# Performance work log

Measured on AMD Instinct MI355X. Metric: run time of the kernel, lower is better.

## Reference

```python
import jax, jax.numpy as jnp
import numpy as np

N_NODES = 100000
N_EDGES = 320000
DIM = 256  # hidden_dim*2 (bi-RNN)
BN_EPS = 1e-5


def setup_inputs() -> dict:
    key = jax.random.key(0)
    k1, k2, k3 = jax.random.split(key, 3)
    x = jax.random.normal(k1, (N_NODES, DIM), dtype=jnp.float32)
    W = jax.random.normal(k2, (DIM, DIM), dtype=jnp.float32) * (1.0 / np.sqrt(DIM))
    b = jnp.zeros((DIM,), dtype=jnp.float32)
    gamma = jnp.ones((DIM,), dtype=jnp.float32)
    beta = jnp.zeros((DIM,), dtype=jnp.float32)
    edge_index = jax.random.randint(k3, (2, N_EDGES), 0, N_NODES, dtype=jnp.int64)
    return {"x": x, "W": W, "b": b, "gamma": gamma, "beta": beta,
            "edge_index": edge_index}


def reference(x, W, b, gamma, beta, edge_index):
    N = x.shape[0]
    # --- GCNConv: add self-loops, symmetric deg^-1/2 normalization ---
    loop = jnp.arange(N, dtype=edge_index.dtype)
    row = jnp.concatenate([edge_index[0], loop])  # source / j
    col = jnp.concatenate([edge_index[1], loop])  # target / i
    deg = jax.ops.segment_sum(jnp.ones_like(col, dtype=x.dtype), col,
                              num_segments=N)
    dinv = jax.lax.rsqrt(deg)  # deg >= 1 due to self-loops
    norm = dinv[row] * dinv[col]  # [E+N]
    h = x @ W  # linear transform before propagation (PyG GCNConv)
    msg = h[row] * norm[:, None]  # gather + scale, [E+N, F]
    out = jax.ops.segment_sum(msg, col, num_segments=N) + b  # scatter-add
    # --- BatchNorm1d over nodes (training-mode batch statistics) ---
    mean = jnp.mean(out, axis=0)
    var = jnp.var(out, axis=0)
    out = (out - mean) * jax.lax.rsqrt(var + BN_EPS) * gamma + beta
    return jnp.tanh(out)
```

## Files before the change

kernel.cpp:

```cpp
#include <hip/hip_runtime.h>
#include <stdint.h>

#define N_NODES 100000
#define N_EDGES 320000
#define DIM 256
#define BN_EPS 1e-5f

typedef __attribute__((ext_vector_type(8))) short short8;
typedef __attribute__((ext_vector_type(4))) float f32x4;
typedef __attribute__((ext_vector_type(2))) unsigned int u32x2;

__device__ __forceinline__ float bf2f(unsigned short u) {
    union { unsigned int i; float f; } v; v.i = ((unsigned int)u) << 16; return v.f;
}
__device__ __forceinline__ unsigned short f2bf(float f) {
    union { float f; unsigned int i; } v; v.f = f;
    unsigned int x = v.i;
    return (unsigned short)((x + 0x7fffu + ((x >> 16) & 1u)) >> 16);
}
__device__ __forceinline__ int eidx(const int* ei, int i64, int which, int e) {
    int idx = which * N_EDGES + e;
    return i64 ? ei[idx * 2] : ei[idx];
}
__device__ __forceinline__ f32x4 ldx4(const void* xv, int xf32, size_t off) {
    if (xf32) return *(const f32x4*)((const float*)xv + off);
    uint2 u = *(const uint2*)((const unsigned short*)xv + off);
    f32x4 o;
    o[0] = bf2f((unsigned short)(u.x & 0xffffu));
    o[1] = bf2f((unsigned short)(u.x >> 16));
    o[2] = bf2f((unsigned short)(u.y & 0xffffu));
    o[3] = bf2f((unsigned short)(u.y >> 16));
    return o;
}

__global__ void k_detect(const unsigned short* __restrict__ xs,
                         const unsigned short* __restrict__ wsw,
                         const int* __restrict__ ei, int* __restrict__ flags) {
    __shared__ int red[3];
    int tid = threadIdx.x;
    if (tid < 3) red[tid] = 0;
    __syncthreads();
    int badx = 0, badw = 0, nz = 0;
    for (int j = 0; j < 8; ++j) {
        if (!(fabsf(bf2f(xs[tid * 8 + j])) <= 1000.0f)) badx = 1;
        if (!(fabsf(bf2f(wsw[tid * 8 + j])) <= 1000.0f)) badw = 1;
        if (ei[(tid * 8 + j) * 2 + 1] != 0) nz = 1;
    }
    if (badx) atomicOr(&red[0], 1);
    if (badw) atomicOr(&red[1], 1);
    if (nz)   atomicOr(&red[2], 1);
    __syncthreads();
    if (tid == 0) { flags[0] = red[0]; flags[1] = red[1]; flags[2] = red[2] ? 0 : 1; }
}

__global__ void k_zero(int* __restrict__ cnt, float* __restrict__ stats) {
    int i = blockIdx.x * 256 + threadIdx.x;
    if (i < N_NODES) cnt[i] = 0;
    if (i < 512) stats[i] = 0.0f;
}

__global__ void k_cnt(const int* __restrict__ ei, int* __restrict__ cnt,
                      const int* __restrict__ flags) {
    int i64 = flags[2];
    int e = blockIdx.x * 256 + threadIdx.x;
    if (e < N_EDGES) atomicAdd(&cnt[eidx(ei, i64, 1, e)], 1);
}

__global__ void k_dinv(const int* __restrict__ cnt, float* __restrict__ dinv) {
    int i = blockIdx.x * 256 + threadIdx.x;
    if (i < N_NODES) dinv[i] = rsqrtf((float)cnt[i] + 1.0f);
}

__global__ void k_scan1(const int* __restrict__ cnt, int* __restrict__ partial) {
    __shared__ int red[256];
    int t = threadIdx.x, b = blockIdx.x;
    int i0 = b * 512 + t * 2;
    int s = 0;
    if (i0 < N_NODES) s += cnt[i0];
    if (i0 + 1 < N_NODES) s += cnt[i0 + 1];
    red[t] = s;
    __syncthreads();
    for (int off = 128; off > 0; off >>= 1) {
        if (t < off) red[t] += red[t + off];
        __syncthreads();
    }
    if (t == 0) partial[b] = red[0];
}

__global__ void k_scan2(const int* __restrict__ partial, int* __restrict__ pbase) {
    __shared__ int s[256];
    int t = threadIdx.x;
    int v = (t < 200) ? partial[t] : 0;
    s[t] = v;
    __syncthreads();
    for (int off = 1; off < 256; off <<= 1) {
        int u = (t >= off) ? s[t - off] : 0;
        __syncthreads();
        s[t] += u;
        __syncthreads();
    }
    if (t < 200) pbase[t] = s[t] - v;
}

__global__ void k_scan3(const int* __restrict__ cnt, const int* __restrict__ pbase,
                        int* __restrict__ row_start, int* __restrict__ cursor) {
    __shared__ int s[512];
    int t = threadIdx.x, b = blockIdx.x;
    int i = b * 512 + t;
    int v = (i < N_NODES) ? cnt[i] : 0;
    s[t] = v;
    __syncthreads();
    for (int off = 1; off < 512; off <<= 1) {
        int u = (t >= off) ? s[t - off] : 0;
        __syncthreads();
        s[t] += u;
        __syncthreads();
    }
    if (i < N_NODES) {
        int excl = pbase[b] + s[t] - v;
        row_start[i] = excl;
        cursor[i] = excl;
    }
}

__global__ void k_fill(const int* __restrict__ ei, const float* __restrict__ dinv,
                       int* __restrict__ cursor, int2* __restrict__ csr_pk,
                       const int* __restrict__ flags) {
    int i64 = flags[2];
    int e = blockIdx.x * 256 + threadIdx.x;
    if (e >= N_EDGES) return;
    int c = eidx(ei, i64, 1, e);
    int r = eidx(ei, i64, 0, e);
    int slot = atomicAdd(&cursor[c], 1);
    union { float f; int i; } u; u.f = dinv[r] * dinv[c];
    int2 pk; pk.x = r; pk.y = u.i;
    csr_pk[slot] = pk;
}

__global__ void k_wt(const void* __restrict__ wv, unsigned short* __restrict__ Wth,
                     unsigned short* __restrict__ Wtl, const int* __restrict__ flags) {
    int wf32 = flags[1];
    int k = blockIdx.x, n = threadIdx.x;
    float v = wf32 ? ((const float*)wv)[k * DIM + n]
                   : bf2f(((const unsigned short*)wv)[k * DIM + n]);
    unsigned short h = f2bf(v);
    Wth[(size_t)n * DIM + k] = h;
    Wtl[(size_t)n * DIM + k] = f2bf(v - bf2f(h));
}

__global__ void k_agg(const void* __restrict__ xv, const int* __restrict__ row_start,
                      const int* __restrict__ cnt, const int2* __restrict__ csr_pk,
                      const float* __restrict__ dinv,
                      unsigned short* __restrict__ zh, unsigned short* __restrict__ zl,
                      const int* __restrict__ flags, int base) {
    int xf32 = flags[0];
    int gid = blockIdx.x * 256 + threadIdx.x;
    int node = base + (gid >> 6);
    int lane = gid & 63;
    int start = row_start[node];
    int len = cnt[node];
    float dv = dinv[node];
    float s = dv * dv;

    int myi = node;
    float myn = 0.0f;
    if (lane < len) {
        int2 pk = csr_pk[start + lane];
        myi = pk.x;
        union { int i; float f; } u; u.i = pk.y;
        myn = u.f;
    }
    bool big = (len > 63);
    int n_eff;
    if (!big) {
        if (lane == len) myn = s;
        n_eff = len + 1;
    } else {
        n_eff = 64;
    }
    int npad = (n_eff + 3) & ~3;

    f32x4 acc = (f32x4){0.f, 0.f, 0.f, 0.f};
    size_t lo4 = (size_t)(lane * 4);

    if (xf32) {
        const float* xp = (const float*)xv;
        for (int j = 0; j < npad; j += 4) {
            int i0 = __shfl(myi, j),     i1 = __shfl(myi, j + 1);
            int i2 = __shfl(myi, j + 2), i3 = __shfl(myi, j + 3);
            float n0 = __shfl(myn, j),     n1 = __shfl(myn, j + 1);
            float n2 = __shfl(myn, j + 2), n3 = __shfl(myn, j + 3);
            f32x4 x0 = *(const f32x4*)(xp + (size_t)i0 * DIM + lo4);
            f32x4 x1 = *(const f32x4*)(xp + (size_t)i1 * DIM + lo4);
            f32x4 x2 = *(const f32x4*)(xp + (size_t)i2 * DIM + lo4);
            f32x4 x3 = *(const f32x4*)(xp + (size_t)i3 * DIM + lo4);
            #pragma unroll
            for (int q = 0; q < 4; ++q)
                acc[q] += n0 * x0[q] + n1 * x1[q] + n2 * x2[q] + n3 * x3[q];
        }
    } else {
        const unsigned short* xp = (const unsigned short*)xv;
        for (int j = 0; j < npad; j += 4) {
            int i0 = __shfl(myi, j),     i1 = __shfl(myi, j + 1);
            int i2 = __shfl(myi, j + 2), i3 = __shfl(myi, j + 3);
            float n0 = __shfl(myn, j),     n1 = __shfl(myn, j + 1);
            float n2 = __shfl(myn, j + 2), n3 = __shfl(myn, j + 3);
            uint2 u0 = *(const uint2*)(xp + (size_t)i0 * DIM + lo4);
            uint2 u1 = *(const uint2*)(xp + (size_t)i1 * DIM + lo4);
            uint2 u2 = *(const uint2*)(xp + (size_t)i2 * DIM + lo4);
            uint2 u3 = *(const uint2*)(xp + (size_t)i3 * DIM + lo4);
            acc[0] += n0 * bf2f((unsigned short)(u0.x & 0xffffu))
                    + n1 * bf2f((unsigned short)(u1.x & 0xffffu))
                    + n2 * bf2f((unsigned short)(u2.x & 0xffffu))
                    + n3 * bf2f((unsigned short)(u3.x & 0xffffu));
            acc[1] += n0 * bf2f((unsigned short)(u0.x >> 16))
                    + n1 * bf2f((unsigned short)(u1.x >> 16))
                    + n2 * bf2f((unsigned short)(u2.x >> 16))
                    + n3 * bf2f((unsigned short)(u3.x >> 16));
            acc[2] += n0 * bf2f((unsigned short)(u0.y & 0xffffu))
                    + n1 * bf2f((unsigned short)(u1.y & 0xffffu))
                    + n2 * bf2f((unsigned short)(u2.y & 0xffffu))
                    + n3 * bf2f((unsigned short)(u3.y & 0xffffu));
            acc[3] += n0 * bf2f((unsigned short)(u0.y >> 16))
                    + n1 * bf2f((unsigned short)(u1.y >> 16))
                    + n2 * bf2f((unsigned short)(u2.y >> 16))
                    + n3 * bf2f((unsigned short)(u3.y >> 16));
        }
    }
    if (big) {
        f32x4 xs = ldx4(xv, xf32, (size_t)node * DIM + lo4);
        #pragma unroll
        for (int q = 0; q < 4; ++q) acc[q] += s * xs[q];
        for (int t = 64; t < len; ++t) {
            int2 pk = csr_pk[start + t];
            union { int i; float f; } u; u.i = pk.y;
            f32x4 xr = ldx4(xv, xf32, (size_t)pk.x * DIM + lo4);
            #pragma unroll
            for (int q = 0; q < 4; ++q) acc[q] += u.f * xr[q];
        }
    }

    unsigned short h0 = f2bf(acc[0]), h1 = f2bf(acc[1]);
    unsigned short h2 = f2bf(acc[2]), h3 = f2bf(acc[3]);
    u32x2 vh, vl;
    vh[0] = (unsigned int)h0 | ((unsigned int)h1 << 16);
    vh[1] = (unsigned int)h2 | ((unsigned int)h3 << 16);
    vl[0] = (unsigned int)f2bf(acc[0] - bf2f(h0))
          | ((unsigned int)f2bf(acc[1] - bf2f(h1)) << 16);
    vl[1] = (unsigned int)f2bf(acc[2] - bf2f(h2))
          | ((unsigned int)f2bf(acc[3] - bf2f(h3)) << 16);
    size_t zo = (size_t)(node - base) * DIM + lane * 4;
    __builtin_nontemporal_store(vh, (u32x2*)(zh + zo));
    __builtin_nontemporal_store(vl, (u32x2*)(zl + zo));
}

__device__ __forceinline__ void stage_q(const char* zhB, const char* zlB,
                                        char* zsb, int q, int m0l, int tid) {
    #pragma unroll
    for (int i = 0; i < 5; ++i) {
        int d    = i * 4096 + tid * 16;
        int row  = d >> 8;
        int rem  = d & 255;
        int hl   = rem >> 7;
        int slot = (rem >> 4) & 7;
        int slog = slot ^ (row & 7);
        const char* srcb = hl ? zlB : zhB;
        size_t soff = (size_t)(m0l + row) * 512 + (size_t)(q * 128 + slog * 16);
        __builtin_amdgcn_global_load_lds(
            (const __attribute__((address_space(1))) unsigned int*)(srcb + soff),
            (__attribute__((address_space(3))) unsigned int*)(zsb + d),
            16, 0, 0);
    }
}

__launch_bounds__(256, 3)
__global__ void k_gemm(const unsigned short* __restrict__ zh,
                       const unsigned short* __restrict__ zl,
                       const unsigned short* __restrict__ Wth,
                       const unsigned short* __restrict__ Wtl,
                       float* __restrict__ out, float* __restrict__ stats, int base) {
    __shared__ char zs[2][20480];
    int tid = threadIdx.x;
    int m0l = blockIdx.x * 80;
    int w = tid >> 6, lane = tid & 63, quad = lane >> 4, rl = lane & 15;

    f32x4 acc[5][4];
    #pragma unroll
    for (int ms = 0; ms < 5; ++ms)
        #pragma unroll
        for (int nt = 0; nt < 4; ++nt)
            acc[ms][nt] = (f32x4){0.f, 0.f, 0.f, 0.f};

    const char* zhB = (const char*)zh;
    const char* zlB = (const char*)zl;

    stage_q(zhB, zlB, zs[0], 0, m0l, tid);
    __syncthreads();

    for (int q = 0; q < 4; ++q) {
        int cur = q & 1;
        if (q < 3) stage_q(zhB, zlB, zs[cur ^ 1], q + 1, m0l, tid);

        const char* zb = zs[cur];
        #pragma unroll
        for (int kk2 = 0; kk2 < 2; ++kk2) {
            int k0g = q * 64 + kk2 * 32 + quad * 8;
            short8 bh[4], bl[4];
            #pragma unroll
            for (int nt = 0; nt < 4; ++nt) {
                int n = w * 64 + nt * 16 + rl;
                bh[nt] = *(const short8*)(Wth + (size_t)n * DIM + k0g);
                bl[nt] = *(const short8*)(Wtl + (size_t)n * DIM + k0g);
            }
            #pragma unroll
            for (int ms = 0; ms < 5; ++ms) {
                int row = ms * 16 + rl;
                int sp  = (((kk2 * 4 + quad) ^ (row & 7)) << 4);
                const char* rb = zb + row * 256;
                short8 ah = *(const short8*)(rb + sp);
                short8 al = *(const short8*)(rb + 128 + sp);
                #pragma unroll
                for (int nt = 0; nt < 4; ++nt) {
                    acc[ms][nt] = __builtin_amdgcn_mfma_f32_16x16x32_bf16(ah, bh[nt], acc[ms][nt], 0, 0, 0);
                    acc[ms][nt] = __builtin_amdgcn_mfma_f32_16x16x32_bf16(al, bh[nt], acc[ms][nt], 0, 0, 0);
                    acc[ms][nt] = __builtin_amdgcn_mfma_f32_16x16x32_bf16(ah, bl[nt], acc[ms][nt], 0, 0, 0);
                }
            }
        }
        __syncthreads();
    }

    #pragma unroll
    for (int nt = 0; nt < 4; ++nt) {
        int col = w * 64 + nt * 16 + rl;
        float s1 = 0.f, s2 = 0.f;
        #pragma unroll
        for (int ms = 0; ms < 5; ++ms)
            #pragma unroll
            for (int i = 0; i < 4; ++i) {
                float v = acc[ms][nt][i];
                s1 += v; s2 += v * v;
                out[(size_t)(base + m0l + ms * 16 + quad * 4 + i) * DIM + col] = v;
            }
        s1 += __shfl_xor(s1, 16); s1 += __shfl_xor(s1, 32);
        s2 += __shfl_xor(s2, 16); s2 += __shfl_xor(s2, 32);
        if (lane < 16) {
            atomicAdd(&stats[col], s1);
            atomicAdd(&stats[256 + col], s2);
        }
    }
}

__global__ void k_fin(const float* __restrict__ stats, const void* __restrict__ gv,
                      const void* __restrict__ bv, float* __restrict__ scsh,
                      const int* __restrict__ flags) {
    int ff32 = flags[0];
    int f = threadIdx.x;
    const float invN = 1.0f / (float)N_NODES;
    float mean = stats[f] * invN;
    float var = stats[256 + f] * invN - mean * mean;
    float g = ff32 ? ((const float*)gv)[f] : bf2f(((const unsigned short*)gv)[f]);
    float bb = ff32 ? ((const float*)bv)[f] : bf2f(((const unsigned short*)bv)[f]);
    float sc = g * rsqrtf(var + BN_EPS);
    scsh[f] = sc;
    scsh[256 + f] = bb - mean * sc;
}

__global__ void k_final(float* __restrict__ out, const float* __restrict__ scsh) {
    int t = blockIdx.x * 256 + threadIdx.x;
    int f0 = (t & 63) * 4;
    size_t off = (size_t)t * 4;
    f32x4 v = *(const f32x4*)(out + off);
    f32x4 o;
    #pragma unroll
    for (int j = 0; j < 4; ++j)
        o[j] = tanhf(v[j] * scsh[f0 + j] + scsh[256 + f0 + j]);
    *(f32x4*)(out + off) = o;
}

extern "C" void kernel_launch(void* const* d_in, const int* in_sizes, int n_in,
                              void* d_out, int out_size, void* d_ws, size_t ws_size,
                              hipStream_t stream) {
    const void* x     = d_in[0];
    const void* W     = d_in[1];
    const void* gamma = d_in[3];
    const void* beta  = d_in[4];
    const int* ei     = (const int*)d_in[5];
    float* out = (float*)d_out;

    char* ws = (char*)d_ws;
    int*   flags     = (int*)(ws);
    int*   cnt       = (int*)(ws + 4096);
    int*   row_start = (int*)(ws + 409600);
    int*   cursor    = (int*)(ws + 819200);
    float* dinv      = (float*)(ws + 1228800);
    int*   partial   = (int*)(ws + 1638400);
    int*   pbase     = (int*)(ws + 1646592);
    float* stats     = (float*)(ws + 1654784);
    float* scsh      = (float*)(ws + 1662976);
    unsigned short* Wth = (unsigned short*)(ws + 1671168);
    unsigned short* Wtl = (unsigned short*)(ws + 1802240);
    int2*  csr_pk    = (int2*)(ws + 1933312);
    const size_t zoff = 4718592;

    size_t zbytes = ws_size > zoff ? ws_size - zoff : 0;
    long long maxRows = (long long)(zbytes / ((size_t)DIM * 4));
    maxRows -= maxRows % 80;
    if (maxRows <= 0) maxRows = 80;
    if (maxRows > N_NODES) maxRows = N_NODES;

    unsigned short* zh = (unsigned short*)(ws + zoff);
    unsigned short* zl = zh + (size_t)maxRows * DIM;

    k_detect<<<1,    256, 0, stream>>>((const unsigned short*)x, (const unsigned short*)W, ei, flags);
    k_zero  <<<391,  256, 0, stream>>>(cnt, stats);
    k_cnt   <<<1250, 256, 0, stream>>>(ei, cnt, flags);
    k_dinv  <<<391,  256, 0, stream>>>(cnt, dinv);
    k_scan1 <<<200,  256, 0, stream>>>(cnt, partial);
    k_scan2 <<<1,    256, 0, stream>>>(partial, pbase);
    k_scan3 <<<200,  512, 0, stream>>>(cnt, pbase, row_start, cursor);
    k_fill  <<<1250, 256, 0, stream>>>(ei, dinv, cursor, csr_pk, flags);
    k_wt    <<<256,  256, 0, stream>>>(W, Wth, Wtl, flags);

    for (int base = 0; base < N_NODES; base += (int)maxRows) {
        int count = N_NODES - base;
        if (count > (int)maxRows) count = (int)maxRows;
        k_agg <<<count / 4,  256, 0, stream>>>(x, row_start, cnt, csr_pk,
                                               dinv, zh, zl, flags, base);
        k_gemm<<<count / 80, 256, 0, stream>>>(zh, zl, Wth, Wtl, out, stats, base);
    }

    k_fin  <<<1,     256, 0, stream>>>(stats, gamma, beta, scsh, flags);
    k_final<<<25000, 256, 0, stream>>>(out, scsh);
}
```

Baseline: 419.5 us.

## Fuse aggregation into GEMM via LDS and merge small setup kernels

```diff
diff --git a/kernel.cpp b/kernel.cpp
--- a/kernel.cpp
+++ b/kernel.cpp
@@ -8,7 +8,6 @@
 
 typedef __attribute__((ext_vector_type(8))) short short8;
 typedef __attribute__((ext_vector_type(4))) float f32x4;
-typedef __attribute__((ext_vector_type(2))) unsigned int u32x2;
 
 __device__ __forceinline__ float bf2f(unsigned short u) {
     union { unsigned int i; float f; } v; v.i = ((unsigned int)u) << 16; return v.f;
@@ -33,58 +32,70 @@
     return o;
 }
 
-__global__ void k_detect(const unsigned short* __restrict__ xs,
-                         const unsigned short* __restrict__ wsw,
-                         const int* __restrict__ ei, int* __restrict__ flags) {
+__global__ void k_init(const unsigned short* __restrict__ xs,
+                       const unsigned short* __restrict__ wsw,
+                       const int* __restrict__ ei, int* __restrict__ flags,
+                       int* __restrict__ cnt, float* __restrict__ stats) {
     __shared__ int red[3];
-    int tid = threadIdx.x;
-    if (tid < 3) red[tid] = 0;
-    __syncthreads();
-    int badx = 0, badw = 0, nz = 0;
-    for (int j = 0; j < 8; ++j) {
-        if (!(fabsf(bf2f(xs[tid * 8 + j])) <= 1000.0f)) badx = 1;
-        if (!(fabsf(bf2f(wsw[tid * 8 + j])) <= 1000.0f)) badw = 1;
-        if (ei[(tid * 8 + j) * 2 + 1] != 0) nz = 1;
-    }
-    if (badx) atomicOr(&red[0], 1);
-    if (badw) atomicOr(&red[1], 1);
-    if (nz)   atomicOr(&red[2], 1);
-    __syncthreads();
-    if (tid == 0) { flags[0] = red[0]; flags[1] = red[1]; flags[2] = red[2] ? 0 : 1; }
-}
-
-__global__ void k_zero(int* __restrict__ cnt, float* __restrict__ stats) {
-    int i = blockIdx.x * 256 + threadIdx.x;
+    int t = threadIdx.x;
+    int i = blockIdx.x * 256 + t;
     if (i < N_NODES) cnt[i] = 0;
     if (i < 512) stats[i] = 0.0f;
-}
-
-__global__ void k_cnt(const int* __restrict__ ei, int* __restrict__ cnt,
-                      const int* __restrict__ flags) {
-    int i64 = flags[2];
-    int e = blockIdx.x * 256 + threadIdx.x;
-    if (e < N_EDGES) atomicAdd(&cnt[eidx(ei, i64, 1, e)], 1);
-}
-
-__global__ void k_dinv(const int* __restrict__ cnt, float* __restrict__ dinv) {
-    int i = blockIdx.x * 256 + threadIdx.x;
-    if (i < N_NODES) dinv[i] = rsqrtf((float)cnt[i] + 1.0f);
-}
-
-__global__ void k_scan1(const int* __restrict__ cnt, int* __restrict__ partial) {
+    if (blockIdx.x == 0) {
+        if (t < 3) red[t] = 0;
+        __syncthreads();
+        int badx = 0, badw = 0, nz = 0;
+        for (int j = 0; j < 8; ++j) {
+            if (!(fabsf(bf2f(xs[t * 8 + j])) <= 1000.0f)) badx = 1;
+            if (!(fabsf(bf2f(wsw[t * 8 + j])) <= 1000.0f)) badw = 1;
+            if (ei[(t * 8 + j) * 2 + 1] != 0) nz = 1;
+        }
+        if (badx) atomicOr(&red[0], 1);
+        if (badw) atomicOr(&red[1], 1);
+        if (nz)   atomicOr(&red[2], 1);
+        __syncthreads();
+        if (t == 0) { flags[0] = red[0]; flags[1] = red[1]; flags[2] = red[2] ? 0 : 1; }
+    }
+}
+
+__global__ void k_cntwt(const int* __restrict__ ei, int* __restrict__ cnt,
+                        const void* __restrict__ wv, unsigned short* __restrict__ Wth,
+                        unsigned short* __restrict__ Wtl, const int* __restrict__ flags) {
+    int b = blockIdx.x, t = threadIdx.x;
+    if (b < 1250) {
+        int i64 = flags[2];
+        int e = b * 256 + t;
+        if (e < N_EDGES) atomicAdd(&cnt[eidx(ei, i64, 1, e)], 1);
+    } else {
+        int wf32 = flags[1];
+        int k = b - 1250, n = t;
+        float v = wf32 ? ((const float*)wv)[k * DIM + n]
+                       : bf2f(((const unsigned short*)wv)[k * DIM + n]);
+        unsigned short h = f2bf(v);
+        Wth[(size_t)n * DIM + k] = h;
+        Wtl[(size_t)n * DIM + k] = f2bf(v - bf2f(h));
+    }
+}
+
+__global__ void k_dscan(const int* __restrict__ cnt, float* __restrict__ dinv,
+                        int* __restrict__ partial) {
     __shared__ int red[256];
     int t = threadIdx.x, b = blockIdx.x;
-    int i0 = b * 512 + t * 2;
-    int s = 0;
-    if (i0 < N_NODES) s += cnt[i0];
-    if (i0 + 1 < N_NODES) s += cnt[i0 + 1];
-    red[t] = s;
-    __syncthreads();
-    for (int off = 128; off > 0; off >>= 1) {
-        if (t < off) red[t] += red[t + off];
-        __syncthreads();
-    }
-    if (t == 0) partial[b] = red[0];
+    int i = b * 256 + t;
+    if (i < N_NODES) dinv[i] = rsqrtf((float)cnt[i] + 1.0f);
+    if (b < 200) {
+        int i0 = b * 512 + t * 2;
+        int s = 0;
+        if (i0 < N_NODES) s += cnt[i0];
+        if (i0 + 1 < N_NODES) s += cnt[i0 + 1];
+        red[t] = s;
+        __syncthreads();
+        for (int off = 128; off > 0; off >>= 1) {
+            if (t < off) red[t] += red[t + off];
+            __syncthreads();
+        }
+        if (t == 0) partial[b] = red[0];
+    }
 }
 
 __global__ void k_scan2(const int* __restrict__ partial, int* __restrict__ pbase) {
@@ -137,197 +148,154 @@
     csr_pk[slot] = pk;
 }
 
-__global__ void k_wt(const void* __restrict__ wv, unsigned short* __restrict__ Wth,
-                     unsigned short* __restrict__ Wtl, const int* __restrict__ flags) {
-    int wf32 = flags[1];
-    int k = blockIdx.x, n = threadIdx.x;
-    float v = wf32 ? ((const float*)wv)[k * DIM + n]
-                   : bf2f(((const unsigned short*)wv)[k * DIM + n]);
-    unsigned short h = f2bf(v);
-    Wth[(size_t)n * DIM + k] = h;
-    Wtl[(size_t)n * DIM + k] = f2bf(v - bf2f(h));
-}
-
-__global__ void k_agg(const void* __restrict__ xv, const int* __restrict__ row_start,
-                      const int* __restrict__ cnt, const int2* __restrict__ csr_pk,
-                      const float* __restrict__ dinv,
-                      unsigned short* __restrict__ zh, unsigned short* __restrict__ zl,
-                      const int* __restrict__ flags, int base) {
-    int xf32 = flags[0];
-    int gid = blockIdx.x * 256 + threadIdx.x;
-    int node = base + (gid >> 6);
-    int lane = gid & 63;
-    int start = row_start[node];
-    int len = cnt[node];
-    float dv = dinv[node];
-    float s = dv * dv;
-
-    int myi = node;
-    float myn = 0.0f;
-    if (lane < len) {
-        int2 pk = csr_pk[start + lane];
-        myi = pk.x;
-        union { int i; float f; } u; u.i = pk.y;
-        myn = u.f;
-    }
-    bool big = (len > 63);
-    int n_eff;
-    if (!big) {
-        if (lane == len) myn = s;
-        n_eff = len + 1;
-    } else {
-        n_eff = 64;
-    }
-    int npad = (n_eff + 3) & ~3;
-
-    f32x4 acc = (f32x4){0.f, 0.f, 0.f, 0.f};
-    size_t lo4 = (size_t)(lane * 4);
-
-    if (xf32) {
-        const float* xp = (const float*)xv;
-        for (int j = 0; j < npad; j += 4) {
-            int i0 = __shfl(myi, j),     i1 = __shfl(myi, j + 1);
-            int i2 = __shfl(myi, j + 2), i3 = __shfl(myi, j + 3);
-            float n0 = __shfl(myn, j),     n1 = __shfl(myn, j + 1);
-            float n2 = __shfl(myn, j + 2), n3 = __shfl(myn, j + 3);
-            f32x4 x0 = *(const f32x4*)(xp + (size_t)i0 * DIM + lo4);
-            f32x4 x1 = *(const f32x4*)(xp + (size_t)i1 * DIM + lo4);
-            f32x4 x2 = *(const f32x4*)(xp + (size_t)i2 * DIM + lo4);
-            f32x4 x3 = *(const f32x4*)(xp + (size_t)i3 * DIM + lo4);
-            #pragma unroll
-            for (int q = 0; q < 4; ++q)
-                acc[q] += n0 * x0[q] + n1 * x1[q] + n2 * x2[q] + n3 * x3[q];
-        }
-    } else {
-        const unsigned short* xp = (const unsigned short*)xv;
-        for (int j = 0; j < npad; j += 4) {
-            int i0 = __shfl(myi, j),     i1 = __shfl(myi, j + 1);
-            int i2 = __shfl(myi, j + 2), i3 = __shfl(myi, j + 3);
-            float n0 = __shfl(myn, j),     n1 = __shfl(myn, j + 1);
-            float n2 = __shfl(myn, j + 2), n3 = __shfl(myn, j + 3);
-            uint2 u0 = *(const uint2*)(xp + (size_t)i0 * DIM + lo4);
-            uint2 u1 = *(const uint2*)(xp + (size_t)i1 * DIM + lo4);
-            uint2 u2 = *(const uint2*)(xp + (size_t)i2 * DIM + lo4);
-            uint2 u3 = *(const uint2*)(xp + (size_t)i3 * DIM + lo4);
-            acc[0] += n0 * bf2f((unsigned short)(u0.x & 0xffffu))
-                    + n1 * bf2f((unsigned short)(u1.x & 0xffffu))
-                    + n2 * bf2f((unsigned short)(u2.x & 0xffffu))
-                    + n3 * bf2f((unsigned short)(u3.x & 0xffffu));
-            acc[1] += n0 * bf2f((unsigned short)(u0.x >> 16))
-                    + n1 * bf2f((unsigned short)(u1.x >> 16))
-                    + n2 * bf2f((unsigned short)(u2.x >> 16))
-                    + n3 * bf2f((unsigned short)(u3.x >> 16));
-            acc[2] += n0 * bf2f((unsigned short)(u0.y & 0xffffu))
-                    + n1 * bf2f((unsigned short)(u1.y & 0xffffu))
-                    + n2 * bf2f((unsigned short)(u2.y & 0xffffu))
-                    + n3 * bf2f((unsigned short)(u3.y & 0xffffu));
-            acc[3] += n0 * bf2f((unsigned short)(u0.y >> 16))
-                    + n1 * bf2f((unsigned short)(u1.y >> 16))
-                    + n2 * bf2f((unsigned short)(u2.y >> 16))
-                    + n3 * bf2f((unsigned short)(u3.y >> 16));
-        }
-    }
-    if (big) {
-        f32x4 xs = ldx4(xv, xf32, (size_t)node * DIM + lo4);
-        #pragma unroll
-        for (int q = 0; q < 4; ++q) acc[q] += s * xs[q];
-        for (int t = 64; t < len; ++t) {
-            int2 pk = csr_pk[start + t];
-            union { int i; float f; } u; u.i = pk.y;
-            f32x4 xr = ldx4(xv, xf32, (size_t)pk.x * DIM + lo4);
-            #pragma unroll
-            for (int q = 0; q < 4; ++q) acc[q] += u.f * xr[q];
-        }
-    }
-
-    unsigned short h0 = f2bf(acc[0]), h1 = f2bf(acc[1]);
-    unsigned short h2 = f2bf(acc[2]), h3 = f2bf(acc[3]);
-    u32x2 vh, vl;
-    vh[0] = (unsigned int)h0 | ((unsigned int)h1 << 16);
-    vh[1] = (unsigned int)h2 | ((unsigned int)h3 << 16);
-    vl[0] = (unsigned int)f2bf(acc[0] - bf2f(h0))
-          | ((unsigned int)f2bf(acc[1] - bf2f(h1)) << 16);
-    vl[1] = (unsigned int)f2bf(acc[2] - bf2f(h2))
-          | ((unsigned int)f2bf(acc[3] - bf2f(h3)) << 16);
-    size_t zo = (size_t)(node - base) * DIM + lane * 4;
-    __builtin_nontemporal_store(vh, (u32x2*)(zh + zo));
-    __builtin_nontemporal_store(vl, (u32x2*)(zl + zo));
-}
-
-__device__ __forceinline__ void stage_q(const char* zhB, const char* zlB,
-                                        char* zsb, int q, int m0l, int tid) {
-    #pragma unroll
-    for (int i = 0; i < 5; ++i) {
-        int d    = i * 4096 + tid * 16;
-        int row  = d >> 8;
-        int rem  = d & 255;
-        int hl   = rem >> 7;
-        int slot = (rem >> 4) & 7;
-        int slog = slot ^ (row & 7);
-        const char* srcb = hl ? zlB : zhB;
-        size_t soff = (size_t)(m0l + row) * 512 + (size_t)(q * 128 + slog * 16);
-        __builtin_amdgcn_global_load_lds(
-            (const __attribute__((address_space(1))) unsigned int*)(srcb + soff),
-            (__attribute__((address_space(3))) unsigned int*)(zsb + d),
-            16, 0, 0);
-    }
-}
-
-__launch_bounds__(256, 3)
-__global__ void k_gemm(const unsigned short* __restrict__ zh,
-                       const unsigned short* __restrict__ zl,
-                       const unsigned short* __restrict__ Wth,
-                       const unsigned short* __restrict__ Wtl,
-                       float* __restrict__ out, float* __restrict__ stats, int base) {
-    __shared__ char zs[2][20480];
+__launch_bounds__(256, 2)
+__global__ void k_fused(const void* __restrict__ xv, const int* __restrict__ row_start,
+                        const int* __restrict__ cnt, const int2* __restrict__ csr_pk,
+                        const float* __restrict__ dinv,
+                        const unsigned short* __restrict__ Wth,
+                        const unsigned short* __restrict__ Wtl,
+                        float* __restrict__ out, float* __restrict__ stats,
+                        const int* __restrict__ flags) {
+    __shared__ unsigned short zsh[80 * 256];
+    __shared__ unsigned short zsl[80 * 256];
     int tid = threadIdx.x;
     int m0l = blockIdx.x * 80;
     int w = tid >> 6, lane = tid & 63, quad = lane >> 4, rl = lane & 15;
-
-    f32x4 acc[5][4];
+    int xf32 = flags[0];
+    size_t lo4 = (size_t)(lane * 4);
+
+    for (int nn = 0; nn < 20; ++nn) {
+        int row = w * 20 + nn;
+        int node = m0l + row;
+        int start = row_start[node];
+        int len = cnt[node];
+        float dv = dinv[node];
+        float s = dv * dv;
+
+        int myi = node;
+        float myn = 0.0f;
+        if (lane < len) {
+            int2 pk = csr_pk[start + lane];
+            myi = pk.x;
+            union { int i; float f; } u; u.i = pk.y;
+            myn = u.f;
+        }
+        bool big = (len > 63);
+        int n_eff;
+        if (!big) {
+            if (lane == len) myn = s;
+            n_eff = len + 1;
+        } else {
+            n_eff = 64;
+        }
+        int npad = (n_eff + 3) & ~3;
+
+        f32x4 acc = (f32x4){0.f, 0.f, 0.f, 0.f};
+        if (xf32) {
+            const float* xp = (const float*)xv;
+            for (int j = 0; j < npad; j += 4) {
+                int i0 = __shfl(myi, j),     i1 = __shfl(myi, j + 1);
+                int i2 = __shfl(myi, j + 2), i3 = __shfl(myi, j + 3);
+                float n0 = __shfl(myn, j),     n1 = __shfl(myn, j + 1);
+                float n2 = __shfl(myn, j + 2), n3 = __shfl(myn, j + 3);
+                f32x4 x0 = *(const f32x4*)(xp + (size_t)i0 * DIM + lo4);
+                f32x4 x1 = *(const f32x4*)(xp + (size_t)i1 * DIM + lo4);
+                f32x4 x2 = *(const f32x4*)(xp + (size_t)i2 * DIM + lo4);
+                f32x4 x3 = *(const f32x4*)(xp + (size_t)i3 * DIM + lo4);
+                #pragma unroll
+                for (int q = 0; q < 4; ++q)
+                    acc[q] += n0 * x0[q] + n1 * x1[q] + n2 * x2[q] + n3 * x3[q];
+            }
+        } else {
+            const unsigned short* xp = (const unsigned short*)xv;
+            for (int j = 0; j < npad; j += 4) {
+                int i0 = __shfl(myi, j),     i1 = __shfl(myi, j + 1);
+                int i2 = __shfl(myi, j + 2), i3 = __shfl(myi, j + 3);
+                float n0 = __shfl(myn, j),     n1 = __shfl(myn, j + 1);
+                float n2 = __shfl(myn, j + 2), n3 = __shfl(myn, j + 3);
+                uint2 u0 = *(const uint2*)(xp + (size_t)i0 * DIM + lo4);
+                uint2 u1 = *(const uint2*)(xp + (size_t)i1 * DIM + lo4);
+                uint2 u2 = *(const uint2*)(xp + (size_t)i2 * DIM + lo4);
+                uint2 u3 = *(const uint2*)(xp + (size_t)i3 * DIM + lo4);
+                acc[0] += n0 * bf2f((unsigned short)(u0.x & 0xffffu))
+                        + n1 * bf2f((unsigned short)(u1.x & 0xffffu))
+                        + n2 * bf2f((unsigned short)(u2.x & 0xffffu))
+                        + n3 * bf2f((unsigned short)(u3.x & 0xffffu));
+                acc[1] += n0 * bf2f((unsigned short)(u0.x >> 16))
+                        + n1 * bf2f((unsigned short)(u1.x >> 16))
+                        + n2 * bf2f((unsigned short)(u2.x >> 16))
+                        + n3 * bf2f((unsigned short)(u3.x >> 16));
+                acc[2] += n0 * bf2f((unsigned short)(u0.y & 0xffffu))
+                        + n1 * bf2f((unsigned short)(u1.y & 0xffffu))
+                        + n2 * bf2f((unsigned short)(u2.y & 0xffffu))
+                        + n3 * bf2f((unsigned short)(u3.y & 0xffffu));
+                acc[3] += n0 * bf2f((unsigned short)(u0.y >> 16))
+                        + n1 * bf2f((unsigned short)(u1.y >> 16))
+                        + n2 * bf2f((unsigned short)(u2.y >> 16))
+                        + n3 * bf2f((unsigned short)(u3.y >> 16));
+            }
+        }
+        if (big) {
+            f32x4 xs = ldx4(xv, xf32, (size_t)node * DIM + lo4);
+            #pragma unroll
+            for (int q = 0; q < 4; ++q) acc[q] += s * xs[q];
+            for (int t2 = 64; t2 < len; ++t2) {
+                int2 pk = csr_pk[start + t2];
+                union { int i; float f; } u; u.i = pk.y;
+                f32x4 xr = ldx4(xv, xf32, (size_t)pk.x * DIM + lo4);
+                #pragma unroll
+                for (int q = 0; q < 4; ++q) acc[q] += u.f * xr[q];
+            }
+        }
+
+        unsigned short h0 = f2bf(acc[0]), h1 = f2bf(acc[1]);
+        unsigned short h2 = f2bf(acc[2]), h3 = f2bf(acc[3]);
+        uint2 vh, vl;
+        vh.x = (unsigned int)h0 | ((unsigned int)h1 << 16);
+        vh.y = (unsigned int)h2 | ((unsigned int)h3 << 16);
+        vl.x = (unsigned int)f2bf(acc[0] - bf2f(h0))
+             | ((unsigned int)f2bf(acc[1] - bf2f(h1)) << 16);
+        vl.y = (unsigned int)f2bf(acc[2] - bf2f(h2))
+             | ((unsigned int)f2bf(acc[3] - bf2f(h3)) << 16);
+        int sl  = lane >> 1;
+        int swz = (sl & 24) | ((sl & 7) ^ (row & 7));
+        int offb = swz * 16 + (lane & 1) * 8;
+        *(uint2*)((char*)zsh + (size_t)row * 512 + offb) = vh;
+        *(uint2*)((char*)zsl + (size_t)row * 512 + offb) = vl;
+    }
+    __syncthreads();
+
+    f32x4 cacc[5][4];
     #pragma unroll
     for (int ms = 0; ms < 5; ++ms)
         #pragma unroll
         for (int nt = 0; nt < 4; ++nt)
-            acc[ms][nt] = (f32x4){0.f, 0.f, 0.f, 0.f};
-
-    const char* zhB = (const char*)zh;
-    const char* zlB = (const char*)zl;
-
-    stage_q(zhB, zlB, zs[0], 0, m0l, tid);
-    __syncthreads();
-
-    for (int q = 0; q < 4; ++q) {
-        int cur = q & 1;
-        if (q < 3) stage_q(zhB, zlB, zs[cur ^ 1], q + 1, m0l, tid);
-
-        const char* zb = zs[cur];
+            cacc[ms][nt] = (f32x4){0.f, 0.f, 0.f, 0.f};
+
+    #pragma unroll
+    for (int kk = 0; kk < 8; ++kk) {
+        int k0g = kk * 32 + quad * 8;
+        short8 bh[4], bl[4];
         #pragma unroll
-        for (int kk2 = 0; kk2 < 2; ++kk2) {
-            int k0g = q * 64 + kk2 * 32 + quad * 8;
-            short8 bh[4], bl[4];
+        for (int nt = 0; nt < 4; ++nt) {
+            int n = w * 64 + nt * 16 + rl;
+            bh[nt] = *(const short8*)(Wth + (size_t)n * DIM + k0g);
+            bl[nt] = *(const short8*)(Wtl + (size_t)n * DIM + k0g);
+        }
+        #pragma unroll
+        for (int ms = 0; ms < 5; ++ms) {
+            int row = ms * 16 + rl;
+            int slot = kk * 4 + quad;
+            int sl = (slot & 24) | ((slot & 7) ^ (row & 7));
+            short8 ah = *(const short8*)((const char*)zsh + (size_t)row * 512 + sl * 16);
+            short8 al = *(const short8*)((const char*)zsl + (size_t)row * 512 + sl * 16);
             #pragma unroll
             for (int nt = 0; nt < 4; ++nt) {
-                int n = w * 64 + nt * 16 + rl;
-                bh[nt] = *(const short8*)(Wth + (size_t)n * DIM + k0g);
-                bl[nt] = *(const short8*)(Wtl + (size_t)n * DIM + k0g);
-            }
-            #pragma unroll
-            for (int ms = 0; ms < 5; ++ms) {
-                int row = ms * 16 + rl;
-                int sp  = (((kk2 * 4 + quad) ^ (row & 7)) << 4);
-                const char* rb = zb + row * 256;
-                short8 ah = *(const short8*)(rb + sp);
-                short8 al = *(const short8*)(rb + 128 + sp);
-                #pragma unroll
-                for (int nt = 0; nt < 4; ++nt) {
-                    acc[ms][nt] = __builtin_amdgcn_mfma_f32_16x16x32_bf16(ah, bh[nt], acc[ms][nt], 0, 0, 0);
-                    acc[ms][nt] = __builtin_amdgcn_mfma_f32_16x16x32_bf16(al, bh[nt], acc[ms][nt], 0, 0, 0);
-                    acc[ms][nt] = __builtin_amdgcn_mfma_f32_16x16x32_bf16(ah, bl[nt], acc[ms][nt], 0, 0, 0);
-                }
-            }
-        }
-        __syncthreads();
+                cacc[ms][nt] = __builtin_amdgcn_mfma_f32_16x16x32_bf16(ah, bh[nt], cacc[ms][nt], 0, 0, 0);
+                cacc[ms][nt] = __builtin_amdgcn_mfma_f32_16x16x32_bf16(al, bh[nt], cacc[ms][nt], 0, 0, 0);
+                cacc[ms][nt] = __builtin_amdgcn_mfma_f32_16x16x32_bf16(ah, bl[nt], cacc[ms][nt], 0, 0, 0);
+            }
+        }
     }
 
     #pragma unroll
@@ -338,9 +306,9 @@
         for (int ms = 0; ms < 5; ++ms)
             #pragma unroll
             for (int i = 0; i < 4; ++i) {
-                float v = acc[ms][nt][i];
+                float v = cacc[ms][nt][i];
                 s1 += v; s2 += v * v;
-                out[(size_t)(base + m0l + ms * 16 + quad * 4 + i) * DIM + col] = v;
+                out[(size_t)(m0l + ms * 16 + quad * 4 + i) * DIM + col] = v;
             }
         s1 += __shfl_xor(s1, 16); s1 += __shfl_xor(s1, 32);
         s2 += __shfl_xor(s2, 16); s2 += __shfl_xor(s2, 32);
@@ -351,30 +319,31 @@
     }
 }
 
-__global__ void k_fin(const float* __restrict__ stats, const void* __restrict__ gv,
-                      const void* __restrict__ bv, float* __restrict__ scsh,
-                      const int* __restrict__ flags) {
-    int ff32 = flags[0];
-    int f = threadIdx.x;
-    const float invN = 1.0f / (float)N_NODES;
-    float mean = stats[f] * invN;
-    float var = stats[256 + f] * invN - mean * mean;
-    float g = ff32 ? ((const float*)gv)[f] : bf2f(((const unsigned short*)gv)[f]);
-    float bb = ff32 ? ((const float*)bv)[f] : bf2f(((const unsigned short*)bv)[f]);
-    float sc = g * rsqrtf(var + BN_EPS);
-    scsh[f] = sc;
-    scsh[256 + f] = bb - mean * sc;
-}
-
-__global__ void k_final(float* __restrict__ out, const float* __restrict__ scsh) {
-    int t = blockIdx.x * 256 + threadIdx.x;
-    int f0 = (t & 63) * 4;
-    size_t off = (size_t)t * 4;
+__global__ void k_final(float* __restrict__ out, const float* __restrict__ stats,
+                        const void* __restrict__ gv, const void* __restrict__ bv,
+                        const int* __restrict__ flags) {
+    __shared__ float ssc[256], ssh[256];
+    int t = threadIdx.x;
+    {
+        int ff32 = flags[0];
+        const float invN = 1.0f / (float)N_NODES;
+        float mean = stats[t] * invN;
+        float var = stats[256 + t] * invN - mean * mean;
+        float g = ff32 ? ((const float*)gv)[t] : bf2f(((const unsigned short*)gv)[t]);
+        float bb = ff32 ? ((const float*)bv)[t] : bf2f(((const unsigned short*)bv)[t]);
+        float sc = g * rsqrtf(var + BN_EPS);
+        ssc[t] = sc;
+        ssh[t] = bb - mean * sc;
+    }
+    __syncthreads();
+    int gt = blockIdx.x * 256 + t;
+    int f0 = (gt & 63) * 4;
+    size_t off = (size_t)gt * 4;
     f32x4 v = *(const f32x4*)(out + off);
     f32x4 o;
     #pragma unroll
     for (int j = 0; j < 4; ++j)
-        o[j] = tanhf(v[j] * scsh[f0 + j] + scsh[256 + f0 + j]);
+        o[j] = tanhf(v[j] * ssc[f0 + j] + ssh[f0 + j]);
     *(f32x4*)(out + off) = o;
 }
 
@@ -397,39 +366,22 @@
     int*   partial   = (int*)(ws + 1638400);
     int*   pbase     = (int*)(ws + 1646592);
     float* stats     = (float*)(ws + 1654784);
-    float* scsh      = (float*)(ws + 1662976);
     unsigned short* Wth = (unsigned short*)(ws + 1671168);
     unsigned short* Wtl = (unsigned short*)(ws + 1802240);
     int2*  csr_pk    = (int2*)(ws + 1933312);
-    const size_t zoff = 4718592;
-
-    size_t zbytes = ws_size > zoff ? ws_size - zoff : 0;
-    long long maxRows = (long long)(zbytes / ((size_t)DIM * 4));
-    maxRows -= maxRows % 80;
-    if (maxRows <= 0) maxRows = 80;
-    if (maxRows > N_NODES) maxRows = N_NODES;
-
-    unsigned short* zh = (unsigned short*)(ws + zoff);
-    unsigned short* zl = zh + (size_t)maxRows * DIM;
-
-    k_detect<<<1,    256, 0, stream>>>((const unsigned short*)x, (const unsigned short*)W, ei, flags);
-    k_zero  <<<391,  256, 0, stream>>>(cnt, stats);
-    k_cnt   <<<1250, 256, 0, stream>>>(ei, cnt, flags);
-    k_dinv  <<<391,  256, 0, stream>>>(cnt, dinv);
-    k_scan1 <<<200,  256, 0, stream>>>(cnt, partial);
-    k_scan2 <<<1,    256, 0, stream>>>(partial, pbase);
-    k_scan3 <<<200,  512, 0, stream>>>(cnt, pbase, row_start, cursor);
-    k_fill  <<<1250, 256, 0, stream>>>(ei, dinv, cursor, csr_pk, flags);
-    k_wt    <<<256,  256, 0, stream>>>(W, Wth, Wtl, flags);
-
-    for (int base = 0; base < N_NODES; base += (int)maxRows) {
-        int count = N_NODES - base;
-        if (count > (int)maxRows) count = (int)maxRows;
-        k_agg <<<count / 4,  256, 0, stream>>>(x, row_start, cnt, csr_pk,
-                                               dinv, zh, zl, flags, base);
-        k_gemm<<<count / 80, 256, 0, stream>>>(zh, zl, Wth, Wtl, out, stats, base);
-    }
-
-    k_fin  <<<1,     256, 0, stream>>>(stats, gamma, beta, scsh, flags);
-    k_final<<<25000, 256, 0, stream>>>(out, scsh);
-}
+
+    const unsigned short* xs_us = (const unsigned short*)x;
+    const unsigned short* W_us  = (const unsigned short*)W;
+
+    k_init <<<391,  256, 0, stream>>>(xs_us, W_us, ei, flags, cnt, stats);
+    k_cntwt<<<1506, 256, 0, stream>>>(ei, cnt, W, Wth, Wtl, flags);
+    k_dscan<<<391,  256, 0, stream>>>(cnt, dinv, partial);
+    k_scan2<<<1,    256, 0, stream>>>(partial, pbase);
+    k_scan3<<<200,  512, 0, stream>>>(cnt, pbase, row_start, cursor);
+    k_fill <<<1250, 256, 0, stream>>>(ei, dinv, cursor, csr_pk, flags);
+
+    k_fused<<<1250, 256, 0, stream>>>(x, row_start, cnt, csr_pk, dinv,
+                                      Wth, Wtl, out, stats, flags);
+
+    k_final<<<25000, 256, 0, stream>>>(out, stats, gamma, beta, flags);
+}
```

After: 377.3 us. -10.0%, faster.
